# Kernel optimization log

Measured on AMD Instinct MI355X. Metric: run time of the kernel, lower is better.

The kernel has to match this reference:

```python
import jax, jax.numpy as jnp
import numpy as np

PATCH_NUMS = (10, 20, 30, 40)   # action_dim=10 * (1,2,3,4)
L = sum(PATCH_NUMS)             # 100
FIRST_L = PATCH_NUMS[0]         # 10
C = 768; NH = 12; HD = C // NH; DEPTH = 8; V = 4096; CVAE = 32; OBS = 23; TO = 1
EPS = 1e-6
STD = 0.02

LVL = np.concatenate([np.full(pn, i, dtype=np.int64) for i, pn in enumerate(PATCH_NUMS)])  # [L]
ATTN_BIAS = np.where(LVL[:, None] >= LVL[None, :], 0.0, -np.inf).astype(np.float32)       # [L, L] block-causal


def _ln(x):
    # LayerNorm without affine (eps=1e-6), as in norm_layer(..., elementwise_affine=False)
    m = x.mean(-1, keepdims=True)
    v = ((x - m) ** 2).mean(-1, keepdims=True)
    return (x - m) / jnp.sqrt(v + EPS)


def setup_inputs() -> dict:
    key = jax.random.key(0)
    ks = iter(jax.random.split(key, 40))
    B = 128
    p = {}
    p["nobs"] = jax.random.normal(next(ks), (B, TO, OBS), jnp.float32)
    p["x_BLCv_wo_first_l"] = jax.random.normal(next(ks), (B, L - FIRST_L, CVAE), jnp.float32)
    p["obs_w"] = jax.random.normal(next(ks), (OBS * TO, C), jnp.float32) * STD
    p["obs_b"] = jnp.zeros((C,), jnp.float32)
    p["word_w"] = jax.random.normal(next(ks), (CVAE, C), jnp.float32) * STD
    p["word_b"] = jnp.zeros((C,), jnp.float32)
    p["pos_start"] = jax.random.normal(next(ks), (1, FIRST_L, C), jnp.float32) * STD
    p["pos_1LC"] = jax.random.normal(next(ks), (1, L, C), jnp.float32) * STD
    p["lvl_emb"] = jax.random.normal(next(ks), (len(PATCH_NUMS), C), jnp.float32) * STD
    p["ada_w"] = jax.random.normal(next(ks), (DEPTH, C, 6 * C), jnp.float32) * STD
    p["ada_b"] = jnp.zeros((DEPTH, 6 * C), jnp.float32)
    p["qkv_w"] = jax.random.normal(next(ks), (DEPTH, C, 3 * C), jnp.float32) * STD
    p["qkv_b"] = jnp.zeros((DEPTH, 3 * C), jnp.float32)
    p["proj_w"] = jax.random.normal(next(ks), (DEPTH, C, C), jnp.float32) * STD
    p["proj_b"] = jnp.zeros((DEPTH, C), jnp.float32)
    p["fc1_w"] = jax.random.normal(next(ks), (DEPTH, C, 4 * C), jnp.float32) * STD
    p["fc1_b"] = jnp.zeros((DEPTH, 4 * C), jnp.float32)
    p["fc2_w"] = jax.random.normal(next(ks), (DEPTH, 4 * C, C), jnp.float32) * STD
    p["fc2_b"] = jnp.zeros((DEPTH, C), jnp.float32)
    p["hnm_w"] = jax.random.normal(next(ks), (C, 2 * C), jnp.float32) * STD
    p["hnm_b"] = jnp.zeros((2 * C,), jnp.float32)
    p["head_w"] = jax.random.normal(next(ks), (C, V), jnp.float32) * STD
    p["head_b"] = jnp.zeros((V,), jnp.float32)
    return p


def reference(nobs, x_BLCv_wo_first_l, obs_w, obs_b, word_w, word_b, pos_start, pos_1LC,
              lvl_emb, ada_w, ada_b, qkv_w, qkv_b, proj_w, proj_b, fc1_w, fc1_b,
              fc2_w, fc2_b, hnm_w, hnm_b, head_w, head_b):
    B = x_BLCv_wo_first_l.shape[0]
    feat = nobs[:, :TO].reshape(B, -1)                     # [B, obs_dim*To]
    cond = feat @ obs_w + obs_b                            # [B, C] (= sos = cond_BD)
    sos = cond[:, None, :] + pos_start                     # [B, first_l, C]
    x = jnp.concatenate([sos, x_BLCv_wo_first_l @ word_w + word_b], axis=1)  # [B, L, C]
    x = x + lvl_emb[jnp.asarray(LVL)][None] + pos_1LC      # lvl + positional embed
    bias = jnp.asarray(ATTN_BIAS)                          # [L, L]
    cond_s = jax.nn.silu(cond)                             # shared SiLU input to each block's ada_lin
    scale = HD ** -0.5
    for i in range(DEPTH):
        ada = (cond_s @ ada_w[i] + ada_b[i]).reshape(B, 1, 6, C)
        g1, g2, s1, s2, sh1, sh2 = (ada[:, :, j] for j in range(6))
        h = _ln(x) * (s1 + 1.0) + sh1
        qkv = (h @ qkv_w[i] + qkv_b[i]).reshape(B, L, 3, NH, HD)
        q, k, v = qkv[:, :, 0], qkv[:, :, 1], qkv[:, :, 2]
        att = jnp.einsum('bqhd,bkhd->bhqk', q, k) * scale
        att = jax.nn.softmax(att + bias, axis=-1)
        o = jnp.einsum('bhqk,bkhd->bqhd', att, v).reshape(B, L, C)
        x = x + (o @ proj_w[i] + proj_b[i]) * g1
        h = _ln(x) * (s2 + 1.0) + sh2
        h = jax.nn.gelu(h @ fc1_w[i] + fc1_b[i]) @ fc2_w[i] + fc2_b[i]
        x = x + h * g2
    # AdaLNBeforeHead + head
    hd = (cond_s @ hnm_w + hnm_b).reshape(B, 1, 2, C)
    x = _ln(x) * (hd[:, :, 0] + 1.0) + hd[:, :, 1]
    return x @ head_w + head_b                             # [B, L, V]
```

## Files before the change

kernel.cpp:

```cpp
#include <hip/hip_runtime.h>
#include <hip/hip_bf16.h>

typedef unsigned short u16;
typedef unsigned int u32;
typedef __attribute__((ext_vector_type(8))) short bf16x8;
typedef __attribute__((ext_vector_type(4))) float f32x4;

#define GLDS(gptr, lptr) __builtin_amdgcn_global_load_lds( \
    (const __attribute__((address_space(1))) u32*)(gptr), \
    (__attribute__((address_space(3))) u32*)(lptr), 16, 0, 0)

__device__ __forceinline__ float bf2f(u16 x) {
  union { float f; u32 u; } c; c.u = ((u32)x) << 16; return c.f;
}
__device__ __forceinline__ u16 f2bf(float f) {
  union { float f; u32 u; } c; c.f = f;
  u32 u = c.u;
  return (u16)((u + 0x7FFFu + ((u >> 16) & 1u)) >> 16);
}
__device__ __forceinline__ uint2 pack_bf4(f32x4 v) {
  uint2 pk;
  pk.x = ((u32)f2bf(v[1]) << 16) | (u32)f2bf(v[0]);
  pk.y = ((u32)f2bf(v[3]) << 16) | (u32)f2bf(v[2]);
  return pk;
}
__device__ __forceinline__ float gelu1(float v) {
  float t = 0.7978845608028654f * (v + 0.044715f * v * v * v);
  t = fminf(fmaxf(t, -15.f), 15.f);
  float e = __expf(2.f * t);
  return 0.5f * v * (1.f + (e - 1.f) / (e + 1.f));
}

template<int EPI>
__global__ __launch_bounds__(256)
void gemm_kernel(const u16* __restrict__ A, const u16* __restrict__ Bt,
                 const float* __restrict__ bias,
                 u16* __restrict__ outb, float* __restrict__ outf,
                 float* __restrict__ xres, const float* __restrict__ gate, int gstride,
                 int M, int N, int K)
{
  __shared__ u16 ldsA[2][128 * 32];
  __shared__ u16 ldsB[2][128 * 32];
  const int tid = threadIdx.x;
  const int nX = N >> 7;

  int nwg = gridDim.x;
  int orig = blockIdx.x;
  int q = nwg >> 3, r = nwg & 7;
  int xcd = orig & 7, jj = orig >> 3;
  int wg = (xcd < r ? xcd * (q + 1) : r * (q + 1) + (xcd - r) * q) + jj;
  const int m0 = (wg / nX) << 7;
  const int n0 = (wg % nX) << 7;

  const int wid = tid >> 6, lane = tid & 63;
  const int wm = wid >> 1, wn = wid & 1;
  const int lr = lane & 15, lg = lane >> 4;

  f32x4 acc[4][4];
  #pragma unroll
  for (int i = 0; i < 4; ++i)
    #pragma unroll
    for (int j = 0; j < 4; ++j)
      acc[i][j] = (f32x4){0.f, 0.f, 0.f, 0.f};

  const int KT = K >> 5;
  int cur = 0;

  #define STAGE(buf, kt) do { \
    int k0_ = (kt) << 5; \
    _Pragma("unroll") \
    for (int iss = 0; iss < 2; ++iss) { \
      int f_ = iss * 256 + tid; \
      int row_ = f_ >> 2, gl_ = f_ & 3; \
      int g_ = gl_ ^ (row_ & 3); \
      GLDS(A + (size_t)(m0 + row_) * K + k0_ + g_ * 8, &ldsA[buf][f_ * 8]); \
      GLDS(Bt + (size_t)(n0 + row_) * K + k0_ + g_ * 8, &ldsB[buf][f_ * 8]); \
    } \
  } while (0)

  STAGE(0, 0);
  __syncthreads();
  for (int kt = 0; kt < KT; ++kt) {
    if (kt + 1 < KT) STAGE(cur ^ 1, kt + 1);
    bf16x8 af[4], bfr[4];
    #pragma unroll
    for (int i = 0; i < 4; ++i) {
      int ra = wm * 64 + i * 16 + lr;
      af[i] = *(const bf16x8*)&ldsA[cur][(ra * 4 + (lg ^ (ra & 3))) * 8];
      int rb = wn * 64 + i * 16 + lr;
      bfr[i] = *(const bf16x8*)&ldsB[cur][(rb * 4 + (lg ^ (rb & 3))) * 8];
    }
    #pragma unroll
    for (int mi = 0; mi < 4; ++mi)
      #pragma unroll
      for (int ni = 0; ni < 4; ++ni)
        acc[mi][ni] = __builtin_amdgcn_mfma_f32_16x16x32_bf16(bfr[ni], af[mi], acc[mi][ni], 0, 0, 0);
    __syncthreads();
    cur ^= 1;
  }
  #undef STAGE

  f32x4 b4[4];
  #pragma unroll
  for (int ni = 0; ni < 4; ++ni)
    b4[ni] = *(const f32x4*)&bias[n0 + wn * 64 + ni * 16 + lg * 4];

  #pragma unroll
  for (int mi = 0; mi < 4; ++mi) {
    int row = m0 + wm * 64 + mi * 16 + lr;
    int bb = row / 100;
    #pragma unroll
    for (int ni = 0; ni < 4; ++ni) {
      int col = n0 + wn * 64 + ni * 16 + lg * 4;
      f32x4 v = acc[mi][ni] + b4[ni];
      size_t idx = (size_t)row * N + col;
      if (EPI == 0) {
        *(f32x4*)&outf[idx] = v;
      } else if (EPI == 1) {
        *(uint2*)&outb[idx] = pack_bf4(v);
      } else if (EPI == 2) {
        f32x4 g;
        #pragma unroll
        for (int e = 0; e < 4; ++e) g[e] = gelu1(v[e]);
        *(uint2*)&outb[idx] = pack_bf4(g);
      } else {
        f32x4 g4 = *(const f32x4*)&gate[(size_t)bb * gstride + col];
        f32x4 xr = *(f32x4*)&xres[idx];
        xr += v * g4;
        *(f32x4*)&xres[idx] = xr;
      }
    }
  }
}

template<int EPI>
__global__ __launch_bounds__(512, 2)
void gemm256_kernel(const u16* __restrict__ A, const u16* __restrict__ Bt,
                    const float* __restrict__ bias,
                    u16* __restrict__ outb, float* __restrict__ outf,
                    float* __restrict__ xres, const float* __restrict__ gate, int gstride,
                    int M, int N, int K)
{
  extern __shared__ u16 lds[];
  u16* ldsA = lds;
  u16* ldsB = lds + 32768;
  const int tid = threadIdx.x;
  const int nX = N >> 8;

  int nwg = gridDim.x;
  int orig = blockIdx.x;
  int q = nwg >> 3, r = nwg & 7;
  int xcd = orig & 7, jj = orig >> 3;
  int wg = (xcd < r ? xcd * (q + 1) : r * (q + 1) + (xcd - r) * q) + jj;
  const int m0 = (wg / nX) << 8;
  const int n0 = (wg % nX) << 8;

  const int wid = tid >> 6, lane = tid & 63;
  const int wm = wid >> 2, wn = wid & 3;
  const int lr = lane & 15, lg = lane >> 4;

  const u16* Ag = A + (size_t)m0 * K;
  const u16* Bg = Bt + (size_t)n0 * K;

  f32x4 acc[8][4];
  #pragma unroll
  for (int i = 0; i < 8; ++i)
    #pragma unroll
    for (int j = 0; j < 4; ++j)
      acc[i][j] = (f32x4){0.f, 0.f, 0.f, 0.f};

  const int KT = K >> 6;

  #define ISSUE(ldsbase, G, buf, t1, kk) do { \
    int k0_ = ((t1) << 6) + ((kk) << 5); \
    _Pragma("unroll") \
    for (int is_ = 0; is_ < 2; ++is_) { \
      int j_ = is_ * 512 + tid; \
      int row_ = j_ >> 2, gl_ = j_ & 3; \
      int gs_ = gl_ ^ (row_ & 3); \
      GLDS((G) + (size_t)row_ * K + k0_ + gs_ * 8, \
           (ldsbase) + (((((buf) * 2 + (kk)) << 10)) + j_) * 8); \
    } \
  } while (0)

  #define RDA(dst, buf, kk, mf) do { \
    int r_ = wm * 128 + (mf) * 16 + lr; \
    dst = *(const bf16x8*)&ldsA[(((((buf) * 2 + (kk)) << 10)) + r_ * 4 + (lg ^ (r_ & 3))) * 8]; \
  } while (0)
  #define RDB(dst, buf, kk, nf) do { \
    int r_ = wn * 64 + (nf) * 16 + lr; \
    dst = *(const bf16x8*)&ldsB[(((((buf) * 2 + (kk)) << 10)) + r_ * 4 + (lg ^ (r_ & 3))) * 8]; \
  } while (0)

  ISSUE(ldsA, Ag, 0, 0, 0);
  ISSUE(ldsB, Bg, 0, 0, 0);
  ISSUE(ldsA, Ag, 0, 0, 1);
  ISSUE(ldsB, Bg, 0, 0, 1);

  for (int t = 0; t < KT; ++t) {
    const int c = t & 1;
    const bool pf = (t + 1) < KT;
    bf16x8 af[4], bv[4];

    asm volatile("s_waitcnt vmcnt(4)" ::: "memory");
    __builtin_amdgcn_s_barrier();
    if (pf) { ISSUE(ldsA, Ag, c ^ 1, t + 1, 0); }
    RDA(af[0], c, 0, 0); RDA(af[1], c, 0, 1); RDA(af[2], c, 0, 2); RDA(af[3], c, 0, 3);
    RDB(bv[0], c, 0, 0); RDB(bv[1], c, 0, 1); RDB(bv[2], c, 0, 2); RDB(bv[3], c, 0, 3);
    __builtin_amdgcn_s_setprio(1);
    #pragma unroll
    for (int i = 0; i < 4; ++i)
      #pragma unroll
      for (int j = 0; j < 4; ++j)
        acc[i][j] = __builtin_amdgcn_mfma_f32_16x16x32_bf16(bv[j], af[i], acc[i][j], 0, 0, 0);
    __builtin_amdgcn_s_setprio(0);

    __builtin_amdgcn_s_barrier();
    if (pf) { ISSUE(ldsB, Bg, c ^ 1, t + 1, 0); }
    RDA(af[0], c, 0, 4); RDA(af[1], c, 0, 5); RDA(af[2], c, 0, 6); RDA(af[3], c, 0, 7);
    __builtin_amdgcn_s_setprio(1);
    #pragma unroll
    for (int i = 0; i < 4; ++i)
      #pragma unroll
      for (int j = 0; j < 4; ++j)
        acc[4 + i][j] = __builtin_amdgcn_mfma_f32_16x16x32_bf16(bv[j], af[i], acc[4 + i][j], 0, 0, 0);
    __builtin_amdgcn_s_setprio(0);

    if (pf) { asm volatile("s_waitcnt vmcnt(4)" ::: "memory"); }
    else    { asm volatile("s_waitcnt vmcnt(0)" ::: "memory"); }
    __builtin_amdgcn_s_barrier();
    if (pf) { ISSUE(ldsA, Ag, c ^ 1, t + 1, 1); }
    RDA(af[0], c, 1, 0); RDA(af[1], c, 1, 1); RDA(af[2], c, 1, 2); RDA(af[3], c, 1, 3);
    RDB(bv[0], c, 1, 0); RDB(bv[1], c, 1, 1); RDB(bv[2], c, 1, 2); RDB(bv[3], c, 1, 3);
    __builtin_amdgcn_s_setprio(1);
    #pragma unroll
    for (int i = 0; i < 4; ++i)
      #pragma unroll
      for (int j = 0; j < 4; ++j)
        acc[i][j] = __builtin_amdgcn_mfma_f32_16x16x32_bf16(bv[j], af[i], acc[i][j], 0, 0, 0);
    __builtin_amdgcn_s_setprio(0);

    __builtin_amdgcn_s_barrier();
    if (pf) { ISSUE(ldsB, Bg, c ^ 1, t + 1, 1); }
    RDA(af[0], c, 1, 4); RDA(af[1], c, 1, 5); RDA(af[2], c, 1, 6); RDA(af[3], c, 1, 7);
    __builtin_amdgcn_s_setprio(1);
    #pragma unroll
    for (int i = 0; i < 4; ++i)
      #pragma unroll
      for (int j = 0; j < 4; ++j)
        acc[4 + i][j] = __builtin_amdgcn_mfma_f32_16x16x32_bf16(bv[j], af[i], acc[4 + i][j], 0, 0, 0);
    __builtin_amdgcn_s_setprio(0);
  }
  #undef ISSUE
  #undef RDA
  #undef RDB

  f32x4 b4[4];
  #pragma unroll
  for (int nf = 0; nf < 4; ++nf)
    b4[nf] = *(const f32x4*)&bias[n0 + wn * 64 + nf * 16 + lg * 4];

  #pragma unroll
  for (int mf = 0; mf < 8; ++mf) {
    int row = m0 + wm * 128 + mf * 16 + lr;
    int bb = row / 100;
    #pragma unroll
    for (int nf = 0; nf < 4; ++nf) {
      int col = n0 + wn * 64 + nf * 16 + lg * 4;
      f32x4 v = acc[mf][nf] + b4[nf];
      size_t idx = (size_t)row * N + col;
      if (EPI == 0) {
        *(f32x4*)&outf[idx] = v;
      } else if (EPI == 1) {
        *(uint2*)&outb[idx] = pack_bf4(v);
      } else if (EPI == 2) {
        f32x4 g;
        #pragma unroll
        for (int e = 0; e < 4; ++e) g[e] = gelu1(v[e]);
        *(uint2*)&outb[idx] = pack_bf4(g);
      } else {
        f32x4 g4 = *(const f32x4*)&gate[(size_t)bb * gstride + col];
        f32x4 xr = *(f32x4*)&xres[idx];
        xr += v * g4;
        *(f32x4*)&xres[idx] = xr;
      }
    }
  }
}

template<int E>
static inline void launch256(const u16* A, const u16* Bt, const float* bias,
                             u16* ob, float* of, float* xr, const float* gt, int gs,
                             int M, int N, int K, hipStream_t s)
{
  (void)hipFuncSetAttribute(reinterpret_cast<const void*>(&gemm256_kernel<E>),
                            hipFuncAttributeMaxDynamicSharedMemorySize, 131072);
  int nwg = (M >> 8) * (N >> 8);
  gemm256_kernel<E><<<nwg, 512, 131072, s>>>(A, Bt, bias, ob, of, xr, gt, gs, M, N, K);
}

__global__ __launch_bounds__(256)
void attn_kernel(const u16* __restrict__ qkv, u16* __restrict__ o)
{
  __shared__ u16 Qs[896 * 8];
  __shared__ u16 Ks[896 * 8];
  __shared__ u16 Vt[1024 * 8];
  __shared__ u16 Pl[4][256 * 8];
  const int tid = threadIdx.x;
  const int b = blockIdx.x / 12;
  const int h = blockIdx.x % 12;
  const int wid = tid >> 6, lane = tid & 63;
  const int lr = lane & 15, lg = lane >> 4;
  const size_t qbase = (size_t)b * 100 * 2304 + h * 64;

  #pragma unroll
  for (int i = 0; i < 16; ++i)
    ((u32*)Pl)[i * 256 + tid] = 0u;

  for (int it = 0; it < 3; ++it) {
    int idx = it * 256 + tid;
    int row = idx >> 3, gl = idx & 7;
    int g = gl ^ (row & 7);
    int sr = row < 100 ? row : 99;
    const u16* gq = qkv + qbase + (size_t)sr * 2304 + g * 8;
    GLDS(gq, &Qs[idx * 8]);
    GLDS(gq + 768, &Ks[idx * 8]);
  }
  if (tid < 128) {
    int idx = 768 + tid;
    int row = idx >> 3, gl = idx & 7;
    int g = gl ^ (row & 7);
    int sr = row < 100 ? row : 99;
    const u16* gq = qkv + qbase + (size_t)sr * 2304 + g * 8;
    GLDS(gq, &Qs[idx * 8]);
    GLDS(gq + 768, &Ks[idx * 8]);
  }

  for (int it = 0; it < 4; ++it) {
    int idx = it * 256 + tid;
    if (idx < 896) {
      int k = idx >> 3, gd = idx & 7;
      int sk = k < 100 ? k : 99;
      const u16* gv = qkv + qbase + (size_t)sk * 2304 + 1536 + gd * 8;
      u16 vv[8];
      *(uint4*)vv = *(const uint4*)gv;
      #pragma unroll
      for (int e = 0; e < 8; ++e) {
        int d = gd * 8 + e;
        Vt[(d * 16 + ((k >> 3) ^ (d & 15))) * 8 + (k & 7)] = vv[e];
      }
    }
  }
  __syncthreads();

  for (int s = wid; s < 7; s += 4) {
    f32x4 sa[7];
    #pragma unroll
    for (int nt = 0; nt < 7; ++nt) sa[nt] = (f32x4){0.f, 0.f, 0.f, 0.f};
    #pragma unroll
    for (int kk = 0; kk < 2; ++kk) {
      int qrow = s * 16 + lr;
      int qg = kk * 4 + lg;
      bf16x8 qa = *(const bf16x8*)&Qs[(qrow * 8 + (qg ^ (qrow & 7))) * 8];
      #pragma unroll
      for (int nt = 0; nt < 7; ++nt) {
        int krow = nt * 16 + lr;
        bf16x8 kb = *(const bf16x8*)&Ks[(krow * 8 + (qg ^ (krow & 7))) * 8];
        sa[nt] = __builtin_amdgcn_mfma_f32_16x16x32_bf16(qa, kb, sa[nt], 0, 0, 0);
      }
    }
    float pr[7][4];
    #pragma unroll
    for (int r = 0; r < 4; ++r) {
      int qq = s * 16 + lg * 4 + r;
      int kmax = qq < 10 ? 10 : qq < 30 ? 30 : qq < 60 ? 60 : 100;
      float m = -1e30f;
      #pragma unroll
      for (int nt = 0; nt < 7; ++nt) {
        int col = nt * 16 + lr;
        float sv = (col < kmax) ? sa[nt][r] * 0.125f : -1e30f;
        pr[nt][r] = sv;
        m = fmaxf(m, sv);
      }
      m = fmaxf(m, __shfl_xor(m, 1));
      m = fmaxf(m, __shfl_xor(m, 2));
      m = fmaxf(m, __shfl_xor(m, 4));
      m = fmaxf(m, __shfl_xor(m, 8));
      float sum = 0.f;
      #pragma unroll
      for (int nt = 0; nt < 7; ++nt) {
        float e = (pr[nt][r] > -1e29f) ? __expf(pr[nt][r] - m) : 0.f;
        pr[nt][r] = e;
        sum += e;
      }
      sum += __shfl_xor(sum, 1);
      sum += __shfl_xor(sum, 2);
      sum += __shfl_xor(sum, 4);
      sum += __shfl_xor(sum, 8);
      float inv = 1.f / sum;
      #pragma unroll
      for (int nt = 0; nt < 7; ++nt) pr[nt][r] *= inv;
    }
    #pragma unroll
    for (int nt = 0; nt < 7; ++nt) {
      int cg = nt * 2 + (lr >> 3);
      int e = lane & 7;
      #pragma unroll
      for (int r = 0; r < 4; ++r) {
        int row = lg * 4 + r;
        Pl[wid][(row * 16 + (cg ^ row)) * 8 + e] = f2bf(pr[nt][r]);
      }
    }
    asm volatile("s_waitcnt lgkmcnt(0)" ::: "memory");
    f32x4 oa[4];
    #pragma unroll
    for (int i = 0; i < 4; ++i) oa[i] = (f32x4){0.f, 0.f, 0.f, 0.f};
    #pragma unroll
    for (int kk = 0; kk < 4; ++kk) {
      int prow = lr;
      int pg = kk * 4 + lg;
      bf16x8 pa = *(const bf16x8*)&Pl[wid][(prow * 16 + (pg ^ prow)) * 8];
      #pragma unroll
      for (int nt = 0; nt < 4; ++nt) {
        int vrow = nt * 16 + lr;
        bf16x8 vb = *(const bf16x8*)&Vt[(vrow * 16 + (pg ^ (vrow & 15))) * 8];
        oa[nt] = __builtin_amdgcn_mfma_f32_16x16x32_bf16(vb, pa, oa[nt], 0, 0, 0);
      }
    }
    int qq = s * 16 + lr;
    if (qq < 100) {
      #pragma unroll
      for (int nt = 0; nt < 4; ++nt) {
        int d = nt * 16 + lg * 4;
        *(uint2*)&o[(size_t)(b * 100 + qq) * 768 + h * 64 + d] = pack_bf4(oa[nt]);
      }
    }
  }
}

__global__ __launch_bounds__(256)
void transpose_cast(const float* __restrict__ in, u16* __restrict__ out, int K, int N)
{
  __shared__ float tile[32][33];
  size_t zo = (size_t)blockIdx.z * K * N;
  const float* ip = in + zo;
  u16* op = out + zo;
  int n0 = blockIdx.x * 32, k0 = blockIdx.y * 32;
  int tx = threadIdx.x & 31, ty = threadIdx.x >> 5;
  #pragma unroll
  for (int i = 0; i < 32; i += 8)
    tile[ty + i][tx] = ip[(size_t)(k0 + ty + i) * N + n0 + tx];
  __syncthreads();
  #pragma unroll
  for (int i = 0; i < 32; i += 8)
    op[(size_t)(n0 + ty + i) * K + k0 + tx] = f2bf(tile[tx][ty + i]);
}

__global__ __launch_bounds__(256)
void cond_kernel(const float* __restrict__ nobs, const float* __restrict__ obs_w,
                 const float* __restrict__ obs_b, float* __restrict__ cond,
                 u16* __restrict__ cond_s)
{
  int idx = blockIdx.x * 256 + threadIdx.x;
  int b = idx / 768, c = idx - b * 768;
  float acc = obs_b[c];
  #pragma unroll
  for (int i = 0; i < 23; ++i)
    acc += nobs[b * 23 + i] * obs_w[i * 768 + c];
  cond[idx] = acc;
  float sg = acc / (1.f + __expf(-acc));
  cond_s[idx] = f2bf(sg);
}

__global__ __launch_bounds__(256)
void cast_bf16_kernel(const float* __restrict__ in, u16* __restrict__ out, int n)
{
  int idx = blockIdx.x * 256 + threadIdx.x;
  if (idx < n) out[idx] = f2bf(in[idx]);
}

__global__ __launch_bounds__(256)
void build_x_kernel(const float* __restrict__ cond, const float* __restrict__ pos_start,
                    const float* __restrict__ xw, const float* __restrict__ lvl_emb,
                    const float* __restrict__ pos_1LC, float* __restrict__ x)
{
  int idx = blockIdx.x * 256 + threadIdx.x;
  int row = idx / 768, c = idx - row * 768;
  int b = row / 100, l = row - b * 100;
  int lvl = l < 10 ? 0 : l < 30 ? 1 : l < 60 ? 2 : 3;
  float v;
  if (l < 10) v = cond[b * 768 + c] + pos_start[l * 768 + c];
  else        v = xw[(size_t)(b * 90 + (l - 10)) * 768 + c];
  x[idx] = v + lvl_emb[lvl * 768 + c] + pos_1LC[l * 768 + c];
}

__global__ __launch_bounds__(256)
void ln_mod_kernel(const float* __restrict__ x, const float* __restrict__ scale_b,
                   const float* __restrict__ shift_b, int stride, u16* __restrict__ h)
{
  int row = blockIdx.x;
  const float* xr = x + (size_t)row * 768;
  int t = threadIdx.x;
  float v0 = xr[t], v1 = xr[t + 256], v2 = xr[t + 512];
  float s = v0 + v1 + v2;
  float qv = v0 * v0 + v1 * v1 + v2 * v2;
  #pragma unroll
  for (int o = 32; o > 0; o >>= 1) {
    s += __shfl_down(s, o);
    qv += __shfl_down(qv, o);
  }
  __shared__ float red[4][2];
  if ((t & 63) == 0) { red[t >> 6][0] = s; red[t >> 6][1] = qv; }
  __syncthreads();
  float S = red[0][0] + red[1][0] + red[2][0] + red[3][0];
  float Q = red[0][1] + red[1][1] + red[2][1] + red[3][1];
  float mean = S * (1.f / 768.f);
  float var = Q * (1.f / 768.f) - mean * mean;
  float rstd = rsqrtf(var + 1e-6f);
  int bb = row / 100;
  const float* sc = scale_b + (size_t)bb * stride;
  const float* sh = shift_b + (size_t)bb * stride;
  u16* hr = h + (size_t)row * 768;
  hr[t]       = f2bf((v0 - mean) * rstd * (1.f + sc[t])       + sh[t]);
  hr[t + 256] = f2bf((v1 - mean) * rstd * (1.f + sc[t + 256]) + sh[t + 256]);
  hr[t + 512] = f2bf((v2 - mean) * rstd * (1.f + sc[t + 512]) + sh[t + 512]);
}

extern "C" void kernel_launch(void* const* d_in, const int* in_sizes, int n_in,
                              void* d_out, int out_size, void* d_ws, size_t ws_size,
                              hipStream_t stream)
{
  (void)in_sizes; (void)n_in; (void)out_size;
  const float* nobs      = (const float*)d_in[0];
  const float* xv        = (const float*)d_in[1];
  const float* obs_w     = (const float*)d_in[2];
  const float* obs_b     = (const float*)d_in[3];
  const float* word_w    = (const float*)d_in[4];
  const float* word_b    = (const float*)d_in[5];
  const float* pos_start = (const float*)d_in[6];
  const float* pos_1LC   = (const float*)d_in[7];
  const float* lvl_emb   = (const float*)d_in[8];
  const float* ada_w     = (const float*)d_in[9];
  const float* ada_b     = (const float*)d_in[10];
  const float* qkv_w     = (const float*)d_in[11];
  const float* qkv_b     = (const float*)d_in[12];
  const float* proj_w    = (const float*)d_in[13];
  const float* proj_b    = (const float*)d_in[14];
  const float* fc1_w     = (const float*)d_in[15];
  const float* fc1_b     = (const float*)d_in[16];
  const float* fc2_w     = (const float*)d_in[17];
  const float* fc2_b     = (const float*)d_in[18];
  const float* hnm_w     = (const float*)d_in[19];
  const float* hnm_b     = (const float*)d_in[20];
  const float* head_w    = (const float*)d_in[21];
  const float* head_b    = (const float*)d_in[22];
  float* out = (float*)d_out;

  const size_t NEED_BIG = 358000000;
  const bool bigAda = ws_size >= NEED_BIG;
  const int adaStride = bigAda ? 36864 : 4608;

  char* p = (char*)d_ws;
  auto take = [&](size_t bytes) { char* r = p; p += (bytes + 255) & ~(size_t)255; return r; };
  u16* Wword   = (u16*)take((size_t)768 * 32 * 2);
  u16* Wada    = (u16*)take((size_t)8 * 4608 * 768 * 2);
  u16* Wqkv    = (u16*)take((size_t)8 * 2304 * 768 * 2);
  u16* Wproj   = (u16*)take((size_t)8 * 768 * 768 * 2);
  u16* Wfc1    = (u16*)take((size_t)8 * 3072 * 768 * 2);
  u16* Wfc2    = (u16*)take((size_t)8 * 768 * 3072 * 2);
  u16* Whnm    = (u16*)take((size_t)1536 * 768 * 2);
  u16* Whead   = (u16*)take((size_t)4096 * 768 * 2);
  float* condf = (float*)take((size_t)128 * 768 * 4);
  u16* conds   = (u16*)take((size_t)128 * 768 * 2);
  u16* xvb     = (u16*)take((size_t)368640 * 2);
  float* xbuf  = (float*)take((size_t)12800 * 768 * 4);
  u16* hbuf    = (u16*)take((size_t)12800 * 768 * 2);
  float* adab  = (float*)take((size_t)128 * (size_t)adaStride * 4);
  u16* obuf    = (u16*)take((size_t)12800 * 768 * 2);
  float* hdbuf = (float*)take((size_t)128 * 1536 * 4);
  char* big    = take((size_t)12800 * 3072 * 2);
  float* xw  = (float*)big;
  u16* qkvb  = (u16*)big;
  u16* fc1b  = (u16*)big;

  transpose_cast<<<dim3(24, 1, 1),   256, 0, stream>>>(word_w, Wword, 32, 768);
  transpose_cast<<<dim3(144, 24, 8), 256, 0, stream>>>(ada_w,  Wada,  768, 4608);
  transpose_cast<<<dim3(72, 24, 8),  256, 0, stream>>>(qkv_w,  Wqkv,  768, 2304);
  transpose_cast<<<dim3(24, 24, 8),  256, 0, stream>>>(proj_w, Wproj, 768, 768);
  transpose_cast<<<dim3(96, 24, 8),  256, 0, stream>>>(fc1_w,  Wfc1,  768, 3072);
  transpose_cast<<<dim3(24, 96, 8),  256, 0, stream>>>(fc2_w,  Wfc2,  3072, 768);
  transpose_cast<<<dim3(48, 24, 1),  256, 0, stream>>>(hnm_w,  Whnm,  768, 1536);
  transpose_cast<<<dim3(128, 24, 1), 256, 0, stream>>>(head_w, Whead, 768, 4096);

  cond_kernel<<<384, 256, 0, stream>>>(nobs, obs_w, obs_b, condf, conds);
  cast_bf16_kernel<<<1440, 256, 0, stream>>>(xv, xvb, 368640);
  gemm_kernel<0><<<dim3(90 * 6), 256, 0, stream>>>(xvb, Wword, word_b,
      nullptr, xw, nullptr, nullptr, 0, 11520, 768, 32);
  build_x_kernel<<<38400, 256, 0, stream>>>(condf, pos_start, xw, lvl_emb, pos_1LC, xbuf);

  if (bigAda)
    gemm_kernel<0><<<dim3(288), 256, 0, stream>>>(conds, Wada, ada_b,
        nullptr, adab, nullptr, nullptr, 0, 128, 36864, 768);

  for (int i = 0; i < 8; ++i) {
    if (!bigAda)
      gemm_kernel<0><<<dim3(36), 256, 0, stream>>>(conds, Wada + (size_t)i * 4608 * 768,
          ada_b + (size_t)i * 4608, nullptr, adab, nullptr, nullptr, 0, 128, 4608, 768);
    float* adaL = bigAda ? adab + (size_t)i * 4608 : adab;
    ln_mod_kernel<<<12800, 256, 0, stream>>>(xbuf, adaL + 2 * 768, adaL + 4 * 768, adaStride, hbuf);
    launch256<1>(hbuf, Wqkv + (size_t)i * 2304 * 768, qkv_b + (size_t)i * 2304,
                 qkvb, nullptr, nullptr, nullptr, 0, 12800, 2304, 768, stream);
    attn_kernel<<<1536, 256, 0, stream>>>(qkvb, obuf);
    gemm_kernel<3><<<dim3(100 * 6), 256, 0, stream>>>(obuf, Wproj + (size_t)i * 768 * 768,
        proj_b + (size_t)i * 768, nullptr, nullptr, xbuf, adaL + 0 * 768, adaStride, 12800, 768, 768);
    ln_mod_kernel<<<12800, 256, 0, stream>>>(xbuf, adaL + 3 * 768, adaL + 5 * 768, adaStride, hbuf);
    launch256<2>(hbuf, Wfc1 + (size_t)i * 3072 * 768, fc1_b + (size_t)i * 3072,
                 fc1b, nullptr, nullptr, nullptr, 0, 12800, 3072, 768, stream);
    gemm_kernel<3><<<dim3(100 * 6), 256, 0, stream>>>(fc1b, Wfc2 + (size_t)i * 768 * 3072,
        fc2_b + (size_t)i * 768, nullptr, nullptr, xbuf, adaL + 1 * 768, adaStride, 12800, 768, 3072);
  }

  gemm_kernel<0><<<dim3(12), 256, 0, stream>>>(conds, Whnm, hnm_b,
      nullptr, hdbuf, nullptr, nullptr, 0, 128, 1536, 768);
  ln_mod_kernel<<<12800, 256, 0, stream>>>(xbuf, hdbuf, hdbuf + 768, 1536, hbuf);
  launch256<0>(hbuf, Whead, head_b, nullptr, out, nullptr, nullptr, 0,
               12800, 4096, 768, stream);
}
```

Before: 3.598 ms.

## Replace 256x256 GEMM with 128x128 BK=64 kernel across all layer GEMMs

```diff
diff --git a/kernel.cpp b/kernel.cpp
--- a/kernel.cpp
+++ b/kernel.cpp
@@ -33,14 +33,14 @@
 
 template<int EPI>
 __global__ __launch_bounds__(256)
-void gemm_kernel(const u16* __restrict__ A, const u16* __restrict__ Bt,
-                 const float* __restrict__ bias,
-                 u16* __restrict__ outb, float* __restrict__ outf,
-                 float* __restrict__ xres, const float* __restrict__ gate, int gstride,
-                 int M, int N, int K)
-{
-  __shared__ u16 ldsA[2][128 * 32];
-  __shared__ u16 ldsB[2][128 * 32];
+void gemm64_kernel(const u16* __restrict__ A, const u16* __restrict__ Bt,
+                   const float* __restrict__ bias,
+                   u16* __restrict__ outb, float* __restrict__ outf,
+                   float* __restrict__ xres, const float* __restrict__ gate, int gstride,
+                   int M, int N, int K)
+{
+  __shared__ u16 ldsA[2][128 * 64];
+  __shared__ u16 ldsB[2][128 * 64];
   const int tid = threadIdx.x;
   const int nX = N >> 7;
 
@@ -63,42 +63,46 @@
     for (int j = 0; j < 4; ++j)
       acc[i][j] = (f32x4){0.f, 0.f, 0.f, 0.f};
 
-  const int KT = K >> 5;
+  const int KT = K >> 6;
   int cur = 0;
 
-  #define STAGE(buf, kt) do { \
-    int k0_ = (kt) << 5; \
+  #define STAGE64(buf, kt) do { \
+    int k0_ = (kt) << 6; \
     _Pragma("unroll") \
-    for (int iss = 0; iss < 2; ++iss) { \
+    for (int iss = 0; iss < 4; ++iss) { \
       int f_ = iss * 256 + tid; \
-      int row_ = f_ >> 2, gl_ = f_ & 3; \
-      int g_ = gl_ ^ (row_ & 3); \
+      int row_ = f_ >> 3, gl_ = f_ & 7; \
+      int g_ = gl_ ^ (row_ & 7); \
       GLDS(A + (size_t)(m0 + row_) * K + k0_ + g_ * 8, &ldsA[buf][f_ * 8]); \
       GLDS(Bt + (size_t)(n0 + row_) * K + k0_ + g_ * 8, &ldsB[buf][f_ * 8]); \
     } \
   } while (0)
 
-  STAGE(0, 0);
+  STAGE64(0, 0);
   __syncthreads();
   for (int kt = 0; kt < KT; ++kt) {
-    if (kt + 1 < KT) STAGE(cur ^ 1, kt + 1);
-    bf16x8 af[4], bfr[4];
-    #pragma unroll
-    for (int i = 0; i < 4; ++i) {
-      int ra = wm * 64 + i * 16 + lr;
-      af[i] = *(const bf16x8*)&ldsA[cur][(ra * 4 + (lg ^ (ra & 3))) * 8];
-      int rb = wn * 64 + i * 16 + lr;
-      bfr[i] = *(const bf16x8*)&ldsB[cur][(rb * 4 + (lg ^ (rb & 3))) * 8];
-    }
-    #pragma unroll
-    for (int mi = 0; mi < 4; ++mi)
-      #pragma unroll
-      for (int ni = 0; ni < 4; ++ni)
-        acc[mi][ni] = __builtin_amdgcn_mfma_f32_16x16x32_bf16(bfr[ni], af[mi], acc[mi][ni], 0, 0, 0);
+    if (kt + 1 < KT) STAGE64(cur ^ 1, kt + 1);
+    #pragma unroll
+    for (int kk = 0; kk < 2; ++kk) {
+      bf16x8 af[4], bv[4];
+      #pragma unroll
+      for (int i = 0; i < 4; ++i) {
+        int ra = wm * 64 + i * 16 + lr;
+        int da = kk * 4 + lg;
+        af[i] = *(const bf16x8*)&ldsA[cur][(ra * 8 + (da ^ (ra & 7))) * 8];
+        int rb = wn * 64 + i * 16 + lr;
+        bv[i] = *(const bf16x8*)&ldsB[cur][(rb * 8 + (da ^ (rb & 7))) * 8];
+      }
+      #pragma unroll
+      for (int mi = 0; mi < 4; ++mi)
+        #pragma unroll
+        for (int ni = 0; ni < 4; ++ni)
+          acc[mi][ni] = __builtin_amdgcn_mfma_f32_16x16x32_bf16(bv[ni], af[mi], acc[mi][ni], 0, 0, 0);
+    }
     __syncthreads();
     cur ^= 1;
   }
-  #undef STAGE
+  #undef STAGE64
 
   f32x4 b4[4];
   #pragma unroll
@@ -134,140 +138,87 @@
 }
 
 template<int EPI>
-__global__ __launch_bounds__(512, 2)
-void gemm256_kernel(const u16* __restrict__ A, const u16* __restrict__ Bt,
-                    const float* __restrict__ bias,
-                    u16* __restrict__ outb, float* __restrict__ outf,
-                    float* __restrict__ xres, const float* __restrict__ gate, int gstride,
-                    int M, int N, int K)
-{
-  extern __shared__ u16 lds[];
-  u16* ldsA = lds;
-  u16* ldsB = lds + 32768;
+__global__ __launch_bounds__(256)
+void gemm_kernel(const u16* __restrict__ A, const u16* __restrict__ Bt,
+                 const float* __restrict__ bias,
+                 u16* __restrict__ outb, float* __restrict__ outf,
+                 float* __restrict__ xres, const float* __restrict__ gate, int gstride,
+                 int M, int N, int K)
+{
+  __shared__ u16 ldsA[2][128 * 32];
+  __shared__ u16 ldsB[2][128 * 32];
   const int tid = threadIdx.x;
-  const int nX = N >> 8;
+  const int nX = N >> 7;
 
   int nwg = gridDim.x;
   int orig = blockIdx.x;
   int q = nwg >> 3, r = nwg & 7;
   int xcd = orig & 7, jj = orig >> 3;
   int wg = (xcd < r ? xcd * (q + 1) : r * (q + 1) + (xcd - r) * q) + jj;
-  const int m0 = (wg / nX) << 8;
-  const int n0 = (wg % nX) << 8;
+  const int m0 = (wg / nX) << 7;
+  const int n0 = (wg % nX) << 7;
 
   const int wid = tid >> 6, lane = tid & 63;
-  const int wm = wid >> 2, wn = wid & 3;
+  const int wm = wid >> 1, wn = wid & 1;
   const int lr = lane & 15, lg = lane >> 4;
 
-  const u16* Ag = A + (size_t)m0 * K;
-  const u16* Bg = Bt + (size_t)n0 * K;
-
-  f32x4 acc[8][4];
-  #pragma unroll
-  for (int i = 0; i < 8; ++i)
+  f32x4 acc[4][4];
+  #pragma unroll
+  for (int i = 0; i < 4; ++i)
     #pragma unroll
     for (int j = 0; j < 4; ++j)
       acc[i][j] = (f32x4){0.f, 0.f, 0.f, 0.f};
 
-  const int KT = K >> 6;
-
-  #define ISSUE(ldsbase, G, buf, t1, kk) do { \
-    int k0_ = ((t1) << 6) + ((kk) << 5); \
+  const int KT = K >> 5;
+  int cur = 0;
+
+  #define STAGE(buf, kt) do { \
+    int k0_ = (kt) << 5; \
     _Pragma("unroll") \
-    for (int is_ = 0; is_ < 2; ++is_) { \
-      int j_ = is_ * 512 + tid; \
-      int row_ = j_ >> 2, gl_ = j_ & 3; \
-      int gs_ = gl_ ^ (row_ & 3); \
-      GLDS((G) + (size_t)row_ * K + k0_ + gs_ * 8, \
-           (ldsbase) + (((((buf) * 2 + (kk)) << 10)) + j_) * 8); \
+    for (int iss = 0; iss < 2; ++iss) { \
+      int f_ = iss * 256 + tid; \
+      int row_ = f_ >> 2, gl_ = f_ & 3; \
+      int g_ = gl_ ^ (row_ & 3); \
+      GLDS(A + (size_t)(m0 + row_) * K + k0_ + g_ * 8, &ldsA[buf][f_ * 8]); \
+      GLDS(Bt + (size_t)(n0 + row_) * K + k0_ + g_ * 8, &ldsB[buf][f_ * 8]); \
     } \
   } while (0)
 
-  #define RDA(dst, buf, kk, mf) do { \
-    int r_ = wm * 128 + (mf) * 16 + lr; \
-    dst = *(const bf16x8*)&ldsA[(((((buf) * 2 + (kk)) << 10)) + r_ * 4 + (lg ^ (r_ & 3))) * 8]; \
-  } while (0)
-  #define RDB(dst, buf, kk, nf) do { \
-    int r_ = wn * 64 + (nf) * 16 + lr; \
-    dst = *(const bf16x8*)&ldsB[(((((buf) * 2 + (kk)) << 10)) + r_ * 4 + (lg ^ (r_ & 3))) * 8]; \
-  } while (0)
-
-  ISSUE(ldsA, Ag, 0, 0, 0);
-  ISSUE(ldsB, Bg, 0, 0, 0);
-  ISSUE(ldsA, Ag, 0, 0, 1);
-  ISSUE(ldsB, Bg, 0, 0, 1);
-
-  for (int t = 0; t < KT; ++t) {
-    const int c = t & 1;
-    const bool pf = (t + 1) < KT;
-    bf16x8 af[4], bv[4];
-
-    asm volatile("s_waitcnt vmcnt(4)" ::: "memory");
-    __builtin_amdgcn_s_barrier();
-    if (pf) { ISSUE(ldsA, Ag, c ^ 1, t + 1, 0); }
-    RDA(af[0], c, 0, 0); RDA(af[1], c, 0, 1); RDA(af[2], c, 0, 2); RDA(af[3], c, 0, 3);
-    RDB(bv[0], c, 0, 0); RDB(bv[1], c, 0, 1); RDB(bv[2], c, 0, 2); RDB(bv[3], c, 0, 3);
-    __builtin_amdgcn_s_setprio(1);
-    #pragma unroll
-    for (int i = 0; i < 4; ++i)
-      #pragma unroll
-      for (int j = 0; j < 4; ++j)
-        acc[i][j] = __builtin_amdgcn_mfma_f32_16x16x32_bf16(bv[j], af[i], acc[i][j], 0, 0, 0);
-    __builtin_amdgcn_s_setprio(0);
-
-    __builtin_amdgcn_s_barrier();
-    if (pf) { ISSUE(ldsB, Bg, c ^ 1, t + 1, 0); }
-    RDA(af[0], c, 0, 4); RDA(af[1], c, 0, 5); RDA(af[2], c, 0, 6); RDA(af[3], c, 0, 7);
-    __builtin_amdgcn_s_setprio(1);
-    #pragma unroll
-    for (int i = 0; i < 4; ++i)
-      #pragma unroll
-      for (int j = 0; j < 4; ++j)
-        acc[4 + i][j] = __builtin_amdgcn_mfma_f32_16x16x32_bf16(bv[j], af[i], acc[4 + i][j], 0, 0, 0);
-    __builtin_amdgcn_s_setprio(0);
-
-    if (pf) { asm volatile("s_waitcnt vmcnt(4)" ::: "memory"); }
-    else    { asm volatile("s_waitcnt vmcnt(0)" ::: "memory"); }
-    __builtin_amdgcn_s_barrier();
-    if (pf) { ISSUE(ldsA, Ag, c ^ 1, t + 1, 1); }
-    RDA(af[0], c, 1, 0); RDA(af[1], c, 1, 1); RDA(af[2], c, 1, 2); RDA(af[3], c, 1, 3);
-    RDB(bv[0], c, 1, 0); RDB(bv[1], c, 1, 1); RDB(bv[2], c, 1, 2); RDB(bv[3], c, 1, 3);
-    __builtin_amdgcn_s_setprio(1);
-    #pragma unroll
-    for (int i = 0; i < 4; ++i)
-      #pragma unroll
-      for (int j = 0; j < 4; ++j)
-        acc[i][j] = __builtin_amdgcn_mfma_f32_16x16x32_bf16(bv[j], af[i], acc[i][j], 0, 0, 0);
-    __builtin_amdgcn_s_setprio(0);
-
-    __builtin_amdgcn_s_barrier();
-    if (pf) { ISSUE(ldsB, Bg, c ^ 1, t + 1, 1); }
-    RDA(af[0], c, 1, 4); RDA(af[1], c, 1, 5); RDA(af[2], c, 1, 6); RDA(af[3], c, 1, 7);
-    __builtin_amdgcn_s_setprio(1);
-    #pragma unroll
-    for (int i = 0; i < 4; ++i)
-      #pragma unroll
-      for (int j = 0; j < 4; ++j)
-        acc[4 + i][j] = __builtin_amdgcn_mfma_f32_16x16x32_bf16(bv[j], af[i], acc[4 + i][j], 0, 0, 0);
-    __builtin_amdgcn_s_setprio(0);
-  }
-  #undef ISSUE
-  #undef RDA
-  #undef RDB
+  STAGE(0, 0);
+  __syncthreads();
+  for (int kt = 0; kt < KT; ++kt) {
+    if (kt + 1 < KT) STAGE(cur ^ 1, kt + 1);
+    bf16x8 af[4], bfr[4];
+    #pragma unroll
+    for (int i = 0; i < 4; ++i) {
+      int ra = wm * 64 + i * 16 + lr;
+      af[i] = *(const bf16x8*)&ldsA[cur][(ra * 4 + (lg ^ (ra & 3))) * 8];
+      int rb = wn * 64 + i * 16 + lr;
+      bfr[i] = *(const bf16x8*)&ldsB[cur][(rb * 4 + (lg ^ (rb & 3))) * 8];
+    }
+    #pragma unroll
+    for (int mi = 0; mi < 4; ++mi)
+      #pragma unroll
+      for (int ni = 0; ni < 4; ++ni)
+        acc[mi][ni] = __builtin_amdgcn_mfma_f32_16x16x32_bf16(bfr[ni], af[mi], acc[mi][ni], 0, 0, 0);
+    __syncthreads();
+    cur ^= 1;
+  }
+  #undef STAGE
 
   f32x4 b4[4];
   #pragma unroll
-  for (int nf = 0; nf < 4; ++nf)
-    b4[nf] = *(const f32x4*)&bias[n0 + wn * 64 + nf * 16 + lg * 4];
-
-  #pragma unroll
-  for (int mf = 0; mf < 8; ++mf) {
-    int row = m0 + wm * 128 + mf * 16 + lr;
+  for (int ni = 0; ni < 4; ++ni)
+    b4[ni] = *(const f32x4*)&bias[n0 + wn * 64 + ni * 16 + lg * 4];
+
+  #pragma unroll
+  for (int mi = 0; mi < 4; ++mi) {
+    int row = m0 + wm * 64 + mi * 16 + lr;
     int bb = row / 100;
     #pragma unroll
-    for (int nf = 0; nf < 4; ++nf) {
-      int col = n0 + wn * 64 + nf * 16 + lg * 4;
-      f32x4 v = acc[mf][nf] + b4[nf];
+    for (int ni = 0; ni < 4; ++ni) {
+      int col = n0 + wn * 64 + ni * 16 + lg * 4;
+      f32x4 v = acc[mi][ni] + b4[ni];
       size_t idx = (size_t)row * N + col;
       if (EPI == 0) {
         *(f32x4*)&outf[idx] = v;
@@ -286,17 +237,6 @@
       }
     }
   }
-}
-
-template<int E>
-static inline void launch256(const u16* A, const u16* Bt, const float* bias,
-                             u16* ob, float* of, float* xr, const float* gt, int gs,
-                             int M, int N, int K, hipStream_t s)
-{
-  (void)hipFuncSetAttribute(reinterpret_cast<const void*>(&gemm256_kernel<E>),
-                            hipFuncAttributeMaxDynamicSharedMemorySize, 131072);
-  int nwg = (M >> 8) * (N >> 8);
-  gemm256_kernel<E><<<nwg, 512, 131072, s>>>(A, Bt, bias, ob, of, xr, gt, gs, M, N, K);
 }
 
 __global__ __launch_bounds__(256)
@@ -599,30 +539,30 @@
   build_x_kernel<<<38400, 256, 0, stream>>>(condf, pos_start, xw, lvl_emb, pos_1LC, xbuf);
 
   if (bigAda)
-    gemm_kernel<0><<<dim3(288), 256, 0, stream>>>(conds, Wada, ada_b,
+    gemm64_kernel<0><<<dim3(288), 256, 0, stream>>>(conds, Wada, ada_b,
         nullptr, adab, nullptr, nullptr, 0, 128, 36864, 768);
 
   for (int i = 0; i < 8; ++i) {
     if (!bigAda)
-      gemm_kernel<0><<<dim3(36), 256, 0, stream>>>(conds, Wada + (size_t)i * 4608 * 768,
+      gemm64_kernel<0><<<dim3(36), 256, 0, stream>>>(conds, Wada + (size_t)i * 4608 * 768,
           ada_b + (size_t)i * 4608, nullptr, adab, nullptr, nullptr, 0, 128, 4608, 768);
     float* adaL = bigAda ? adab + (size_t)i * 4608 : adab;
     ln_mod_kernel<<<12800, 256, 0, stream>>>(xbuf, adaL + 2 * 768, adaL + 4 * 768, adaStride, hbuf);
-    launch256<1>(hbuf, Wqkv + (size_t)i * 2304 * 768, qkv_b + (size_t)i * 2304,
-                 qkvb, nullptr, nullptr, nullptr, 0, 12800, 2304, 768, stream);
+    gemm64_kernel<1><<<dim3(100 * 18), 256, 0, stream>>>(hbuf, Wqkv + (size_t)i * 2304 * 768,
+        qkv_b + (size_t)i * 2304, qkvb, nullptr, nullptr, nullptr, 0, 12800, 2304, 768);
     attn_kernel<<<1536, 256, 0, stream>>>(qkvb, obuf);
-    gemm_kernel<3><<<dim3(100 * 6), 256, 0, stream>>>(obuf, Wproj + (size_t)i * 768 * 768,
+    gemm64_kernel<3><<<dim3(100 * 6), 256, 0, stream>>>(obuf, Wproj + (size_t)i * 768 * 768,
         proj_b + (size_t)i * 768, nullptr, nullptr, xbuf, adaL + 0 * 768, adaStride, 12800, 768, 768);
     ln_mod_kernel<<<12800, 256, 0, stream>>>(xbuf, adaL + 3 * 768, adaL + 5 * 768, adaStride, hbuf);
-    launch256<2>(hbuf, Wfc1 + (size_t)i * 3072 * 768, fc1_b + (size_t)i * 3072,
-                 fc1b, nullptr, nullptr, nullptr, 0, 12800, 3072, 768, stream);
-    gemm_kernel<3><<<dim3(100 * 6), 256, 0, stream>>>(fc1b, Wfc2 + (size_t)i * 768 * 3072,
+    gemm64_kernel<2><<<dim3(100 * 24), 256, 0, stream>>>(hbuf, Wfc1 + (size_t)i * 3072 * 768,
+        fc1_b + (size_t)i * 3072, fc1b, nullptr, nullptr, nullptr, 0, 12800, 3072, 768);
+    gemm64_kernel<3><<<dim3(100 * 6), 256, 0, stream>>>(fc1b, Wfc2 + (size_t)i * 768 * 3072,
         fc2_b + (size_t)i * 768, nullptr, nullptr, xbuf, adaL + 1 * 768, adaStride, 12800, 768, 3072);
   }
 
   gemm_kernel<0><<<dim3(12), 256, 0, stream>>>(conds, Whnm, hnm_b,
       nullptr, hdbuf, nullptr, nullptr, 0, 128, 1536, 768);
   ln_mod_kernel<<<12800, 256, 0, stream>>>(xbuf, hdbuf, hdbuf + 768, 1536, hbuf);
-  launch256<0>(hbuf, Whead, head_b, nullptr, out, nullptr, nullptr, 0,
-               12800, 4096, 768, stream);
-}
+  gemm64_kernel<0><<<dim3(100 * 32), 256, 0, stream>>>(hbuf, Whead, head_b,
+      nullptr, out, nullptr, nullptr, 0, 12800, 4096, 768);
+}
```

After: 3.260 ms. -9.4%, faster.
